# Performance work log

Measured on AMD Instinct MI355X. Metric: run time of the kernel, lower is better.

Reference implementation:

```python
import jax, jax.numpy as jnp
import numpy as np

B = 8192
D = 128
N_CLASSES = 100
TEMPERATURE = 0.1


def setup_inputs() -> dict:
    key = jax.random.key(0)
    k1, k2 = jax.random.split(key)
    feats = jax.random.normal(k1, (B, D), dtype=jnp.float32)
    # L2-normalise as the docstring assumes
    feats = feats / jnp.linalg.norm(feats, axis=1, keepdims=True)
    labels = jax.random.randint(k2, (B,), 0, N_CLASSES, dtype=jnp.int64)
    return {"features": feats, "labels": labels}


def reference(features, labels):
    features = features.astype(jnp.float32)
    b = features.shape[0]
    sim = (features @ features.T) / TEMPERATURE            # (B, B)
    labels_eq = labels[None, :] == labels[:, None]          # (B, B)
    self_mask = ~jnp.eye(b, dtype=bool)                     # (B, B), False on diag
    pos_mask = labels_eq & self_mask

    sim_max = jax.lax.stop_gradient(jnp.max(sim, axis=1, keepdims=True))
    logits = sim - sim_max                                  # (B, B)
    exp_logits = jnp.exp(logits) * self_mask.astype(jnp.float32)
    log_sum_exp = jnp.log(jnp.sum(exp_logits, axis=1, keepdims=True) + 1e-12)
    log_prob = logits - log_sum_exp                         # (B, B)

    n_positives = jnp.sum(pos_mask.astype(jnp.float32), axis=1)  # (B,)
    valid = n_positives > 0
    mean_log_prob = jnp.sum(pos_mask.astype(jnp.float32) * log_prob, axis=1) \
        / jnp.maximum(n_positives, 1.0)

    valid_f = valid.astype(jnp.float32)
    n_valid = jnp.sum(valid_f)
    loss = -jnp.sum(mean_log_prob * valid_f) / jnp.maximum(n_valid, 1.0)
    # match torch: return 0 if no anchor has a positive
    return jnp.where(n_valid > 0, loss, jnp.float32(0.0))
```

## Files before the change

kernel.cpp:

```cpp
#include <hip/hip_runtime.h>
#include <hip/hip_bf16.h>


#define BB 8192
#define DD 128
#define NC 16
#define COLCHUNK (BB / NC)
#define ITERS (COLCHUNK / 128)
#define TEMP_INV 10.0f
#define MSHIFT 10.5f
#define C1F 14.426950408889634f
#define C2F -15.148297929334116f

typedef __bf16 bf16x8 __attribute__((ext_vector_type(8)));
typedef float floatx4 __attribute__((ext_vector_type(4)));

__device__ inline float fast_exp2(float x) {
#if __has_builtin(__builtin_amdgcn_exp2f)
    return __builtin_amdgcn_exp2f(x);
#else
    return exp2f(x);
#endif
}

__device__ inline unsigned short f2bf(float f) {
    unsigned u = __float_as_uint(f);
    return (unsigned short)((u + 0x7FFFu + ((u >> 16) & 1u)) >> 16);
}

__global__ __launch_bounds__(256) void supcon_convert(
    const void* __restrict__ fin, const void* __restrict__ lin,
    unsigned short* __restrict__ fbf, int* __restrict__ lab,
    float* __restrict__ accbuf)
{
    int lane = threadIdx.x & 63;
    unsigned ue = ((unsigned)((const unsigned short*)fin)[2 * lane]) << 16;
    float fe = __uint_as_float(ue);
    float ve = fe * fe;
    int odd_or = ((const int*)lin)[2 * lane + 1];
#pragma unroll
    for (int m = 1; m < 64; m <<= 1) {
        ve += __shfl_xor(ve, m, 64);
        odd_or |= __shfl_xor(odd_or, m, 64);
    }
    bool f_bf16 = (ve > 0.05f) && (ve < 4.0f);
    bool l_i64  = (odd_or == 0);

    int gid = blockIdx.x * 256 + threadIdx.x;
    if (!f_bf16) {
        float4 v = ((const float4*)fin)[gid];
        ushort4 o;
        o.x = f2bf(v.x); o.y = f2bf(v.y); o.z = f2bf(v.z); o.w = f2bf(v.w);
        ((ushort4*)fbf)[gid] = o;
    } else {
        ((ushort4*)fbf)[gid] = ((const ushort4*)fin)[gid];
    }
    if (blockIdx.x < 32) {
        int li = blockIdx.x * 256 + threadIdx.x;
        const int* L = (const int*)lin;
        lab[li] = l_i64 ? L[2 * li] : L[li];
    }
    if (blockIdx.x == 0 && threadIdx.x == 0) {
        accbuf[0] = 0.0f;
        accbuf[1] = 0.0f;
        ((unsigned*)accbuf)[2] = 0u;
    }
}

__global__ __launch_bounds__(256, 2) void supcon_main(
    const unsigned short* __restrict__ Fb, const int* __restrict__ labels,
    float* __restrict__ e_part, float* __restrict__ p_part,
    float* __restrict__ diag)
{
    __shared__ unsigned char ldsbuf[32768];
    __shared__ float red[2][128][2];

    const int tid  = threadIdx.x;
    const int lane = tid & 63;
    const int wid  = tid >> 6;
    const int wrow = wid >> 1;
    const int wcol = wid & 1;
    const int quad = lane >> 4;
    const int l16  = lane & 15;

    const int chunk   = blockIdx.x;
    const int rowbase = blockIdx.y * 128;
    const int colchunkbase = chunk * COLCHUNK;

    {
        const unsigned char* gA = (const unsigned char*)(Fb) + (size_t)rowbase * 256;
#pragma unroll
        for (int rnd = 0; rnd < 8; ++rnd) {
            int off = rnd * 4096 + tid * 16;
            int row = off >> 8;
            int g   = (off >> 4) & 15;
            int gs  = g ^ (row & 15);
            int4 v  = *(const int4*)(gA + off);
            *(int4*)(&ldsbuf[row * 256 + gs * 16]) = v;
        }
    }
    __syncthreads();

    bf16x8 afrag[4][4];
#pragma unroll
    for (int ti = 0; ti < 4; ++ti) {
        int row = wrow * 64 + ti * 16 + l16;
#pragma unroll
        for (int k = 0; k < 4; ++k) {
            int g  = k * 4 + quad;
            int gs = g ^ (row & 15);
            afrag[ti][k] = *(const bf16x8*)(&ldsbuf[row * 256 + gs * 16]);
        }
    }

    int lab_row[16];
#pragma unroll
    for (int ti = 0; ti < 4; ++ti)
#pragma unroll
        for (int r = 0; r < 4; ++r)
            lab_row[ti * 4 + r] = labels[rowbase + wrow * 64 + ti * 16 + quad * 4 + r];

    float e_acc[16], p_acc[16];
#pragma unroll
    for (int i = 0; i < 16; ++i) { e_acc[i] = 0.0f; p_acc[i] = 0.0f; }

    __syncthreads();

    for (int it = 0; it < ITERS; ++it) {
        int colbase = colchunkbase + it * 128;
        const unsigned char* gB = (const unsigned char*)(Fb) + (size_t)colbase * 256;
#pragma unroll
        for (int rnd = 0; rnd < 8; ++rnd) {
            int off = rnd * 4096 + tid * 16;
            int row = off >> 8;
            int g   = (off >> 4) & 15;
            int gs  = g ^ (row & 15);
            int4 v  = *(const int4*)(gB + off);
            *(int4*)(&ldsbuf[row * 256 + gs * 16]) = v;
        }
        __syncthreads();

#pragma unroll
        for (int tj = 0; tj < 4; ++tj) {
            int coll = wcol * 64 + tj * 16 + l16;
            bf16x8 bfrag[4];
#pragma unroll
            for (int k = 0; k < 4; ++k) {
                int g  = k * 4 + quad;
                int gs = g ^ (coll & 15);
                bfrag[k] = *(const bf16x8*)(&ldsbuf[coll * 256 + gs * 16]);
            }
            floatx4 acc[4];
#pragma unroll
            for (int ti = 0; ti < 4; ++ti) acc[ti] = (floatx4){0.f, 0.f, 0.f, 0.f};
#pragma unroll
            for (int k = 0; k < 4; ++k)
#pragma unroll
                for (int ti = 0; ti < 4; ++ti)
                    acc[ti] = __builtin_amdgcn_mfma_f32_16x16x32_bf16(
                        afrag[ti][k], bfrag[k], acc[ti], 0, 0, 0);

            {
                int ctb = colbase + wcol * 64 + tj * 16;
                unsigned u = (unsigned)(ctb - (rowbase + wrow * 64));
                if (u < 64u) {
#pragma unroll
                    for (int ti2 = 0; ti2 < 4; ++ti2) {
                        if (u == (unsigned)(ti2 * 16)) {
#pragma unroll
                            for (int r = 0; r < 4; ++r)
                                if (l16 == quad * 4 + r)
                                    diag[ctb + l16] = acc[ti2][r];
                        }
                    }
                }
            }

            int lab_c = labels[colbase + coll];
#pragma unroll
            for (int ti = 0; ti < 4; ++ti) {
#pragma unroll
                for (int r = 0; r < 4; ++r) {
                    int i = ti * 4 + r;
                    float a  = acc[ti][r];
                    float ex = fast_exp2(__builtin_fmaf(a, C1F, C2F));
                    e_acc[i] += ex;
                    float peq = (lab_c == lab_row[i]) ? 1.0f : 0.0f;
                    p_acc[i] = __builtin_fmaf(peq, a, p_acc[i]);
                }
            }
        }
        __syncthreads();
    }

#pragma unroll
    for (int i = 0; i < 16; ++i) {
        float e = e_acc[i], p = p_acc[i];
#pragma unroll
        for (int m = 1; m < 16; m <<= 1) {
            e += __shfl_xor(e, m, 64);
            p += __shfl_xor(p, m, 64);
        }
        if (l16 == 0) {
            int row_local = wrow * 64 + (i >> 2) * 16 + quad * 4 + (i & 3);
            red[0][row_local][wcol] = e;
            red[1][row_local][wcol] = p;
        }
    }
    __syncthreads();

    if (tid < 128) {
        size_t idx = (size_t)chunk * BB + (rowbase + tid);
        e_part[idx] = red[0][tid][0] + red[0][tid][1];
        p_part[idx] = red[1][tid][0] + red[1][tid][1];
    }
}

__global__ __launch_bounds__(256) void supcon_reduce(
    const float* __restrict__ e_part, const float* __restrict__ p_part,
    const int* __restrict__ labels, const float* __restrict__ diag,
    float* __restrict__ accbuf, float* __restrict__ out)
{
    __shared__ int cnt[128];
    if (threadIdx.x < 128) cnt[threadIdx.x] = 0;
    __syncthreads();
    for (int i = threadIdx.x; i < BB; i += 256)
        atomicAdd(&cnt[labels[i]], 1);
    __syncthreads();

    int row = blockIdx.x * 256 + threadIdx.x;
    float e = 0.f, p = 0.f;
#pragma unroll
    for (int c = 0; c < NC; ++c) {
        size_t idx = (size_t)c * BB + row;
        e += e_part[idx]; p += p_part[idx];
    }
    float d = diag[row];
    e -= fast_exp2(__builtin_fmaf(d, C1F, C2F));
    p -= d;
    int n_i = cnt[labels[row]] - 1;

    float contrib = 0.f, vld = 0.f;
    if (n_i > 0) {
        vld = 1.0f;
        contrib = -(p * TEMP_INV / (float)n_i - MSHIFT - logf(e));
    }
#pragma unroll
    for (int m = 1; m < 64; m <<= 1) {
        contrib += __shfl_xor(contrib, m, 64);
        vld     += __shfl_xor(vld, m, 64);
    }
    __shared__ float rl[4], rv[4];
    int lane = threadIdx.x & 63, w = threadIdx.x >> 6;
    if (lane == 0) { rl[w] = contrib; rv[w] = vld; }
    __syncthreads();
    if (threadIdx.x == 0) {
        float L = rl[0] + rl[1] + rl[2] + rl[3];
        float V = rv[0] + rv[1] + rv[2] + rv[3];
        atomicAdd(&accbuf[0], L);
        atomicAdd(&accbuf[1], V);
        __threadfence();
        unsigned t = atomicAdd((unsigned*)accbuf + 2, 1u);
        if (t == 31u) {
            float Ls = atomicAdd(&accbuf[0], 0.0f);
            float Vs = atomicAdd(&accbuf[1], 0.0f);
            out[0] = (Vs > 0.5f) ? (Ls / Vs) : 0.0f;
        }
    }
}

extern "C" void kernel_launch(void* const* d_in, const int* in_sizes, int n_in,
                              void* d_out, int out_size, void* d_ws, size_t ws_size,
                              hipStream_t stream)
{
    const void* Fin = d_in[0];
    const void* Lin = d_in[1];

    unsigned short* fbf = (unsigned short*)d_ws;
    int*   lab      = (int*)((char*)d_ws + (size_t)BB * DD * 2);
    float* e_part   = (float*)((char*)lab + (size_t)BB * 4);
    float* p_part   = e_part + (size_t)NC * BB;
    float* diag     = p_part + (size_t)NC * BB;
    float* accbuf   = diag + BB;

    supcon_convert<<<BB * DD / 4 / 256, 256, 0, stream>>>(Fin, Lin, fbf, lab, accbuf);

    dim3 grid(NC, BB / 128);
    supcon_main<<<grid, 256, 0, stream>>>(fbf, lab, e_part, p_part, diag);

    supcon_reduce<<<32, 256, 0, stream>>>(e_part, p_part, lab, diag, accbuf, (float*)d_out);
}
```

Baseline: 98.57 us.

## Load MFMA fragments directly from global memory and double column chunks

Removes the LDS staging of the A and B tiles. Each wave now loads its bf16 fragments straight from global memory into registers, which eliminates the shared-memory writes, swizzling and block-level barriers. The column split NC is also doubled so the grid has more blocks with fewer iterations each. In exchange, B tiles are re-fetched per wave (twice per block) through cache instead of being shared via LDS, so global/L2 traffic rises. The partial-sum buffers and the reduction must also handle twice as many chunks.

```diff
diff --git a/kernel.cpp b/kernel.cpp
--- a/kernel.cpp
+++ b/kernel.cpp
@@ -4,7 +4,7 @@
 
 #define BB 8192
 #define DD 128
-#define NC 16
+#define NC 32
 #define COLCHUNK (BB / NC)
 #define ITERS (COLCHUNK / 128)
 #define TEMP_INV 10.0f
@@ -72,7 +72,6 @@
     float* __restrict__ e_part, float* __restrict__ p_part,
     float* __restrict__ diag)
 {
-    __shared__ unsigned char ldsbuf[32768];
     __shared__ float red[2][128][2];
 
     const int tid  = threadIdx.x;
@@ -87,30 +86,16 @@
     const int rowbase = blockIdx.y * 128;
     const int colchunkbase = chunk * COLCHUNK;
 
-    {
-        const unsigned char* gA = (const unsigned char*)(Fb) + (size_t)rowbase * 256;
-#pragma unroll
-        for (int rnd = 0; rnd < 8; ++rnd) {
-            int off = rnd * 4096 + tid * 16;
-            int row = off >> 8;
-            int g   = (off >> 4) & 15;
-            int gs  = g ^ (row & 15);
-            int4 v  = *(const int4*)(gA + off);
-            *(int4*)(&ldsbuf[row * 256 + gs * 16]) = v;
-        }
-    }
-    __syncthreads();
+    const unsigned char* Fbc = (const unsigned char*)Fb;
 
     bf16x8 afrag[4][4];
 #pragma unroll
     for (int ti = 0; ti < 4; ++ti) {
-        int row = wrow * 64 + ti * 16 + l16;
-#pragma unroll
-        for (int k = 0; k < 4; ++k) {
-            int g  = k * 4 + quad;
-            int gs = g ^ (row & 15);
-            afrag[ti][k] = *(const bf16x8*)(&ldsbuf[row * 256 + gs * 16]);
-        }
+        int row = rowbase + wrow * 64 + ti * 16 + l16;
+        const unsigned char* gA = Fbc + (size_t)row * 256 + quad * 16;
+#pragma unroll
+        for (int k = 0; k < 4; ++k)
+            afrag[ti][k] = *(const bf16x8*)(gA + k * 64);
     }
 
     int lab_row[16];
@@ -124,32 +109,17 @@
 #pragma unroll
     for (int i = 0; i < 16; ++i) { e_acc[i] = 0.0f; p_acc[i] = 0.0f; }
 
-    __syncthreads();
-
     for (int it = 0; it < ITERS; ++it) {
         int colbase = colchunkbase + it * 128;
-        const unsigned char* gB = (const unsigned char*)(Fb) + (size_t)colbase * 256;
-#pragma unroll
-        for (int rnd = 0; rnd < 8; ++rnd) {
-            int off = rnd * 4096 + tid * 16;
-            int row = off >> 8;
-            int g   = (off >> 4) & 15;
-            int gs  = g ^ (row & 15);
-            int4 v  = *(const int4*)(gB + off);
-            *(int4*)(&ldsbuf[row * 256 + gs * 16]) = v;
-        }
-        __syncthreads();
-
 #pragma unroll
         for (int tj = 0; tj < 4; ++tj) {
-            int coll = wcol * 64 + tj * 16 + l16;
+            int coll = colbase + wcol * 64 + tj * 16 + l16;
+            const unsigned char* gB = Fbc + (size_t)coll * 256 + quad * 16;
             bf16x8 bfrag[4];
 #pragma unroll
-            for (int k = 0; k < 4; ++k) {
-                int g  = k * 4 + quad;
-                int gs = g ^ (coll & 15);
-                bfrag[k] = *(const bf16x8*)(&ldsbuf[coll * 256 + gs * 16]);
-            }
+            for (int k = 0; k < 4; ++k)
+                bfrag[k] = *(const bf16x8*)(gB + k * 64);
+
             floatx4 acc[4];
 #pragma unroll
             for (int ti = 0; ti < 4; ++ti) acc[ti] = (floatx4){0.f, 0.f, 0.f, 0.f};
@@ -176,7 +146,7 @@
                 }
             }
 
-            int lab_c = labels[colbase + coll];
+            int lab_c = labels[coll];
 #pragma unroll
             for (int ti = 0; ti < 4; ++ti) {
 #pragma unroll
@@ -190,7 +160,6 @@
                 }
             }
         }
-        __syncthreads();
     }
 
 #pragma unroll
```

Result: slower. 131.1 us (+33.0%).
